# Optimization experiments

Measured on AMD Instinct MI355X. Metric: run time of the kernel, lower is better.

Reference implementation:

```python
import jax, jax.numpy as jnp
import numpy as np

B, S, E, P, H, F = 4, 4096, 256, 32, 8, 1024
DH = E // H
LN_EPS = 1e-5


def setup_inputs() -> dict:
    key = jax.random.key(0)
    ks = jax.random.split(key, 12)
    dt = jnp.float32
    return {
        "src": jax.random.normal(ks[0], (B, S, E), dt),
        "pos_embed": jax.random.normal(ks[1], (B, P, S), dt),
        # learnable positional transform (pos_linear: P -> P)
        "Wpos": jax.random.normal(ks[2], (P, P), dt) * (1.0 / np.sqrt(P)),
        "bpos": jnp.zeros((P,), dt),
        # RBF kernel hyperparameters (ScaleKernel(RBFKernel)) -- positive scalars
        "lengthscale": jnp.full((), 2.0, dt),
        "outputscale": jnp.full((), 1.0, dt),
        # value / output projections of multihead attention
        "Wv": jax.random.normal(ks[3], (E, E), dt) * (1.0 / np.sqrt(E)),
        "bv": jnp.zeros((E,), dt),
        "Wo": jax.random.normal(ks[4], (E, E), dt) * (1.0 / np.sqrt(E)),
        "bo": jnp.zeros((E,), dt),
        # feed-forward
        "W1": jax.random.normal(ks[5], (F, E), dt) * (1.0 / np.sqrt(E)),
        "b1": jnp.zeros((F,), dt),
        "W2": jax.random.normal(ks[6], (E, F), dt) * (1.0 / np.sqrt(F)),
        "b2": jnp.zeros((E,), dt),
        # layer norms
        "ln1_g": jnp.ones((E,), dt), "ln1_b": jnp.zeros((E,), dt),
        "ln2_g": jnp.ones((E,), dt), "ln2_b": jnp.zeros((E,), dt),
    }


def _layer_norm(x, g, b):
    mu = jnp.mean(x, -1, keepdims=True)
    var = jnp.mean(jnp.square(x - mu), -1, keepdims=True)
    return (x - mu) * jax.lax.rsqrt(var + LN_EPS) * g + b


def _rbf_scores(x, lengthscale, outputscale):
    # x: [B, S, P] -> scaled RBF kernel matrix [B, S, S]
    xs = x / lengthscale
    sq = jnp.sum(xs * xs, axis=-1)  # [B, S]
    d2 = sq[:, :, None] + sq[:, None, :] - 2.0 * jnp.einsum('bsp,btp->bst', xs, xs)
    d2 = jnp.maximum(d2, 0.0)
    return outputscale * jnp.exp(-0.5 * d2)


def reference(src, pos_embed, Wpos, bpos, lengthscale, outputscale,
              Wv, bv, Wo, bo, W1, b1, W2, b2, ln1_g, ln1_b, ln2_g, ln2_b):
    b, s, e = src.shape
    # learnable positional transform: [B,P,S] -> [B,S,P] -> linear -> back
    pe = jnp.einsum('bps,op->bos', pos_embed, Wpos) + bpos[None, :, None]  # [B,P,S]
    # GP-kernel attention scores over sequence positions
    scores = _rbf_scores(pe.transpose(0, 2, 1), lengthscale, outputscale)  # [B,S,S]
    attn = jax.nn.softmax(scores, axis=-1)
    # value projection, per-head weighted sum (scores shared across heads)
    v = (src @ Wv.T + bv).reshape(b, s, H, DH)
    ctx = jnp.einsum('bqk,bkhd->bqhd', attn, v).reshape(b, s, e)
    attn_out = ctx @ Wo.T + bo
    x = _layer_norm(src + attn_out, ln1_g, ln1_b)
    ff = jax.nn.relu(x @ W1.T + b1) @ W2.T + b2
    return _layer_norm(x + ff, ln2_g, ln2_b)
```

## Files before the change

### kernel.cpp

```cpp
#include <hip/hip_runtime.h>
#include <stdint.h>

#define BN 4
#define SN 4096
#define EN 256
#define PN 32
#define FN 1024
#define BS (BN*SN)
#define PAUG 64

typedef uint16_t bf16_t;
typedef short v4s  __attribute__((ext_vector_type(4)));
typedef short v8s  __attribute__((ext_vector_type(8)));
typedef __bf16 bf16x8 __attribute__((ext_vector_type(8)));
typedef float v4f   __attribute__((ext_vector_type(4)));
typedef float v16f  __attribute__((ext_vector_type(16)));

#define MFMA16(a,b,c) __builtin_amdgcn_mfma_f32_16x16x32_bf16(a,b,c,0,0,0)
#define MFMA32(a,b,c) __builtin_amdgcn_mfma_f32_32x32x16_bf16(a,b,c,0,0,0)

__device__ __forceinline__ float b2f(bf16_t x){
    uint32_t u = ((uint32_t)x) << 16; float f; __builtin_memcpy(&f, &u, 4); return f;
}
__device__ __forceinline__ bf16_t f2b(float f){
    uint32_t u; __builtin_memcpy(&u, &f, 4);
    u += 0x7FFFu + ((u >> 16) & 1u);
    return (bf16_t)(u >> 16);
}
__device__ __forceinline__ bf16x8 ldb8(const bf16_t* p){
    v8s r = *(const v8s*)p; return __builtin_bit_cast(bf16x8, r);
}
__device__ __forceinline__ bf16x8 ldb8u(const bf16_t* p){
    v4s lo = *(const v4s*)p;
    v4s hi = *(const v4s*)(p + 4);
    v8s r = __builtin_shufflevector(lo, hi, 0,1,2,3,4,5,6,7);
    return __builtin_bit_cast(bf16x8, r);
}
__device__ __forceinline__ float ldsc(const float* p){ return *p; }
__device__ __forceinline__ float ldsc(const bf16_t* p){ return b2f(*p); }
__device__ __forceinline__ void stsc(float* p, float v){ *p = v; }
__device__ __forceinline__ void stsc(bf16_t* p, float v){ *p = f2b(v); }

#if __has_builtin(__builtin_amdgcn_exp2f)
__device__ __forceinline__ float fexp2(float x){ return __builtin_amdgcn_exp2f(x); }
#else
__device__ __forceinline__ float fexp2(float x){ return exp2f(x); }
#endif

#if __has_builtin(__builtin_amdgcn_cvt_pk_bf16_f32)
typedef __bf16 bf16x2 __attribute__((ext_vector_type(2)));
__device__ __forceinline__ uint32_t pkbf16(float a, float b){
    bf16x2 r = __builtin_amdgcn_cvt_pk_bf16_f32(a, b);
    return __builtin_bit_cast(uint32_t, r);
}
#else
__device__ __forceinline__ uint32_t pkbf16(float a, float b){
    return (uint32_t)f2b(a) | ((uint32_t)f2b(b) << 16);
}
#endif

typedef const __attribute__((address_space(1))) uint32_t* glds_gp;
typedef __attribute__((address_space(3))) uint32_t* glds_lp;
__device__ __forceinline__ void glds16(const bf16_t* g, bf16_t* l){
    __builtin_amdgcn_global_load_lds((glds_gp)g, (glds_lp)l, 16, 0, 0);
}

__global__ __launch_bounds__(256) void prep_kernel(
    const float* __restrict__ src, bf16_t* __restrict__ srcb,
    const float* __restrict__ Wv, bf16_t* __restrict__ Wvb,
    const float* __restrict__ Wo, bf16_t* __restrict__ Wob,
    const float* __restrict__ W1, bf16_t* __restrict__ W1b,
    const float* __restrict__ W2, bf16_t* __restrict__ W2b,
    const float* __restrict__ pos, const float* __restrict__ Wp,
    const float* __restrict__ bp,  const float* __restrict__ lsp,
    bf16_t* __restrict__ xk, bf16_t* __restrict__ xq)
{
    __shared__ float Wsh[PN*PN];
    __shared__ float bsh[PN];
    int bid = blockIdx.x;
    int tid = threadIdx.x;

    if (bid < 4736){
        const float* sp; bf16_t* dp; int off;
        if (bid < 4096){ sp = src; dp = srcb; off = (bid*256 + tid)*4; }
        else {
            int i = ((bid - 4096)*256 + tid)*4;
            if      (i <  65536){ sp=Wv; dp=Wvb; off=i; }
            else if (i < 131072){ sp=Wo; dp=Wob; off=i- 65536; }
            else if (i < 393216){ sp=W1; dp=W1b; off=i-131072; }
            else                { sp=W2; dp=W2b; off=i-393216; }
        }
        float4 f = *(const float4*)(sp + off);
        v4s o;
        o.x = (short)f2b(f.x); o.y = (short)f2b(f.y);
        o.z = (short)f2b(f.z); o.w = (short)f2b(f.w);
        *(v4s*)(dp + off) = o;
        return;
    }

    int pb = bid - 4736;
    int b  = pb >> 4;
    int s  = (pb & 15)*256 + tid;

    for (int i = tid; i < PN*PN; i += 256) Wsh[i] = Wp[i];
    if (tid < PN) bsh[tid] = bp[tid];
    __syncthreads();

    float inv_ls = 1.0f / lsp[0];
    const float c1f = 1.4426950408889634f;

    float col[PN];
    #pragma unroll
    for (int p = 0; p < PN; p++) col[p] = pos[((size_t)b*PN + p)*SN + s];

    uint16_t xb[PN], qb[PN];
    float sq = 0.f;
    #pragma unroll 4
    for (int o = 0; o < PN; o++){
        float pe = bsh[o];
        #pragma unroll
        for (int p = 0; p < PN; p++) pe += col[p] * Wsh[o*PN + p];
        float pv = pe * inv_ls;
        uint16_t h = f2b(pv);
        xb[o] = h;
        qb[o] = f2b(c1f * pv);
        float xr = b2f(h);
        sq += xr * xr;
    }

    size_t base = ((size_t)b*SN + s) * PAUG;
    v8s pk[8];
    #pragma unroll
    for (int c = 0; c < 4; c++)
        #pragma unroll
        for (int j = 0; j < 8; j++) ((short*)&pk[c])[j] = (short)xb[c*8 + j];
    #pragma unroll
    for (int c = 4; c < 8; c++)
        #pragma unroll
        for (int j = 0; j < 8; j++) ((short*)&pk[c])[j] = 0;
    ((short*)&pk[4])[0] = (short)f2b(-0.5f * sq);
    ((short*)&pk[4])[1] = (short)0x3F80;
    #pragma unroll
    for (int c = 0; c < 8; c++) *(v8s*)(xk + base + c*8) = pk[c];

    #pragma unroll
    for (int c = 0; c < 4; c++)
        #pragma unroll
        for (int j = 0; j < 8; j++) ((short*)&pk[c])[j] = (short)qb[c*8 + j];
    ((short*)&pk[4])[0] = (short)f2b(c1f);
    ((short*)&pk[4])[1] = (short)f2b(-0.5f * sq * c1f);
    #pragma unroll
    for (int c = 0; c < 8; c++) *(v8s*)(xq + base + c*8) = pk[c];
}

template<int EPI, typename OutT>
__global__ __launch_bounds__(256) void gemm_t(
    const bf16_t* __restrict__ A, const bf16_t* __restrict__ W,
    const float* __restrict__ bias, OutT* __restrict__ out,
    bf16_t* __restrict__ vt, int N, int K)
{
    __shared__ __align__(16) bf16_t At[2][4096];
    __shared__ __align__(16) bf16_t Wt[2][4096];
    int tid = threadIdx.x;
    int lane = tid & 63, wv = tid >> 6, col = lane & 15, quad = lane >> 4;
    int m0 = blockIdx.x * 64, n0 = blockIdx.y * 64;
    int nck = K >> 6;

    int srow = tid >> 3;
    int spc  = (tid & 7) ^ (srow & 7);
    const bf16_t* asrc = A + (size_t)(m0 + srow)*K + spc*8;
    const bf16_t* wsrc = W + (size_t)(n0 + srow)*K + spc*8;

    v4f acc[4];
    #pragma unroll
    for (int t = 0; t < 4; t++) acc[t] = (v4f){0.f,0.f,0.f,0.f};

    glds16(asrc, &At[0][tid*8]);
    glds16(asrc + (size_t)32*K, &At[0][2048 + tid*8]);
    glds16(wsrc, &Wt[0][tid*8]);
    glds16(wsrc + (size_t)32*K, &Wt[0][2048 + tid*8]);
    __syncthreads();

    for (int c = 0; c < nck; c++){
        int cb = c & 1;
        if (c + 1 < nck){
            glds16(asrc + (c+1)*64, &At[cb^1][tid*8]);
            glds16(asrc + (size_t)32*K + (c+1)*64, &At[cb^1][2048 + tid*8]);
            glds16(wsrc + (c+1)*64, &Wt[cb^1][tid*8]);
            glds16(wsrc + (size_t)32*K + (c+1)*64, &Wt[cb^1][2048 + tid*8]);
        }
        #pragma unroll
        for (int kc = 0; kc < 2; kc++){
            int pc = ((kc*4 + quad) ^ (col & 7)) * 8;
            bf16x8 a = ldb8(&At[cb][(wv*16 + col)*64 + pc]);
            #pragma unroll
            for (int t = 0; t < 4; t++){
                bf16x8 b = ldb8(&Wt[cb][(t*16 + col)*64 + pc]);
                acc[t] = MFMA16(a, b, acc[t]);
            }
        }
        __syncthreads();
    }

    float bfv[4];
    #pragma unroll
    for (int t = 0; t < 4; t++) bfv[t] = bias[n0 + t*16 + col];

    if constexpr (EPI == 3){
        __shared__ uint16_t Tsh[64*74];
        #pragma unroll
        for (int r = 0; r < 4; r++)
            #pragma unroll
            for (int t = 0; t < 4; t++)
                Tsh[(wv*16 + quad*4 + r)*74 + t*16 + col] = f2b(acc[t][r] + bfv[t]);
        __syncthreads();
        int e = tid >> 2, sc = tid & 3;
        int b = m0 >> 12;
        int sbat = m0 & (SN-1);
        int eb   = (n0 + e) >> 5;
        int l31e = (n0 + e) & 31;
        int k16  = (sbat >> 4) + sc;
        v8s p0, p1;
        #pragma unroll
        for (int i = 0; i < 8; i++) ((short*)&p0)[i] = (short)Tsh[(sc*16 + i)*74 + e];
        #pragma unroll
        for (int i = 0; i < 8; i++) ((short*)&p1)[i] = (short)Tsh[(sc*16 + 8 + i)*74 + e];
        bf16_t* dst = vt + ((((size_t)b*8 + eb)*256 + k16)*64 + l31e)*8;
        *(v8s*)dst = p0;
        *(v8s*)(dst + 256) = p1;
    } else {
        #pragma unroll
        for (int r = 0; r < 4; r++){
            int row = m0 + wv*16 + quad*4 + r;
            #pragma unroll
            for (int t = 0; t < 4; t++){
                float y = acc[t][r] + bfv[t];
                if constexpr (EPI == 1) y = fmaxf(y, 0.f);
                stsc(out + (size_t)row*N + n0 + t*16 + col, y);
            }
        }
    }
}

template<typename OutT, typename ResT>
__global__ __launch_bounds__(256) void ln_kernel(
    const bf16_t* __restrict__ y, const ResT* __restrict__ res,
    const float* __restrict__ gamma, const float* __restrict__ beta,
    OutT* __restrict__ out)
{
    int tid = threadIdx.x;
    int row = blockIdx.x * 32 + (tid >> 3);
    int l8  = tid & 7;
    size_t base = (size_t)row * EN;
    float v[32];
    float s1 = 0.f, s2 = 0.f;
    #pragma unroll
    for (int i = 0; i < 4; i++){
        int off = l8*8 + i*64;
        v8s a = *(const v8s*)(y + base + off);
        #pragma unroll
        for (int j = 0; j < 8; j++){
            float t = b2f((bf16_t)(uint16_t)a[j]) + ldsc(res + base + off + j);
            v[i*8 + j] = t; s1 += t; s2 += t*t;
        }
    }
    #pragma unroll
    for (int m = 1; m <= 4; m <<= 1){
        s1 += __shfl_xor(s1, m);
        s2 += __shfl_xor(s2, m);
    }
    float mu = s1 * (1.f/256.f);
    float rs = rsqrtf(s2 * (1.f/256.f) - mu*mu + 1e-5f);
    #pragma unroll
    for (int i = 0; i < 4; i++){
        int off = l8*8 + i*64;
        #pragma unroll
        for (int j = 0; j < 8; j++)
            stsc(out + base + off + j, (v[i*8+j]-mu)*rs*gamma[off+j] + beta[off+j]);
    }
}

__global__ __launch_bounds__(512, 2) void attn_kernel(
    const bf16_t* __restrict__ xk, const bf16_t* __restrict__ xq,
    const bf16_t* __restrict__ vf, const float* __restrict__ osp,
    bf16_t* __restrict__ ctx)
{
    __shared__ __align__(16) bf16_t Wtb[2][64*260];
    __shared__ __align__(16) bf16_t Qs[64*64];
    __shared__ float densh[8][64];
    __shared__ float dent[64];

    int tid  = threadIdx.x;
    int lane = tid & 63;
    int wv   = tid >> 6;
    int col  = lane & 15;
    int quad = lane >> 4;
    int l31  = lane & 31;
    int half = lane >> 5;

    int bid = blockIdx.x;
    int b   = (bid & 7) >> 1;
    int qi  = ((bid >> 3) << 1) | (bid & 1);
    int q0  = qi * 64;

    float k2 = 1.4426950408889634f * osp[0];

    const bf16_t* xkb = xk + (size_t)b * SN * PAUG;
    const bf16_t* xqb = xq + (size_t)b * SN * PAUG;
    const bf16_t* vfb = vf + (((size_t)b*8 + wv)*256)*512 + lane*8;

    {
        int qrow = tid >> 3;
        int qpc  = (tid & 7) ^ (qrow & 7);
        glds16(xqb + (size_t)(q0 + qrow)*PAUG + qpc*8, &Qs[tid*8]);
    }

    v16f acc[2];
    #pragma unroll
    for (int qg = 0; qg < 2; qg++)
        #pragma unroll
        for (int i = 0; i < 16; i++) acc[qg][i] = 0.f;
    float den[4] = {0.f, 0.f, 0.f, 0.f};
    const v4f zero = (v4f){0.f,0.f,0.f,0.f};

    bf16x8 kf[2][2];
    #pragma unroll
    for (int kg = 0; kg < 2; kg++)
        #pragma unroll
        for (int h = 0; h < 2; h++)
            kf[kg][h] = ldb8(xkb + (size_t)(wv*32 + kg*16 + col)*PAUG + h*32 + quad*8);

    __syncthreads();

    for (int c = 0; c < 16; c++){
        int cb = c & 1;
        bf16x8 vr[16];
        #pragma unroll
        for (int sk = 0; sk < 16; sk++)
            vr[sk] = ldb8(vfb + (size_t)(c*16 + sk)*512);

        #pragma unroll
        for (int qg = 0; qg < 2; qg++){
            #pragma unroll
            for (int g2 = 0; g2 < 2; g2++){
                int qr = qg*32 + g2*16 + col;
                bf16x8 qa = ldb8(&Qs[qr*64 + ((quad    ) ^ (col & 7))*8]);
                bf16x8 qb = ldb8(&Qs[qr*64 + ((4 + quad) ^ (col & 7))*8]);
                #pragma unroll
                for (int kg = 0; kg < 2; kg++){
                    v4f st = MFMA16(kf[kg][0], qa, zero);
                    st = MFMA16(kf[kg][1], qb, st);
                    #pragma unroll
                    for (int rp = 0; rp < 2; rp++){
                        float w0 = fexp2(fmaf(k2, fexp2(st[rp*2+0]), -k2));
                        float w1 = fexp2(fmaf(k2, fexp2(st[rp*2+1]), -k2));
                        den[qg*2+g2] += w0 + w1;
                        *(uint32_t*)&Wtb[cb][qr*260 + wv*32 + kg*16 + quad*4 + rp*2]
                            = pkbf16(w0, w1);
                    }
                }
            }
        }
        __syncthreads();

        if (c + 1 < 16){
            #pragma unroll
            for (int kg = 0; kg < 2; kg++)
                #pragma unroll
                for (int h = 0; h < 2; h++)
                    kf[kg][h] = ldb8(xkb + (size_t)((c+1)*256 + wv*32 + kg*16 + col)*PAUG
                                     + h*32 + quad*8);
        }

        #pragma unroll
        for (int qg = 0; qg < 2; qg++){
            #pragma unroll
            for (int sk4 = 0; sk4 < 4; sk4++){
                bf16x8 af[4];
                #pragma unroll
                for (int j = 0; j < 4; j++)
                    af[j] = ldb8u(&Wtb[cb][(qg*32 + l31)*260 + (sk4*4 + j)*16 + half*8]);
                #pragma unroll
                for (int j = 0; j < 4; j++)
                    acc[qg] = MFMA32(af[j], vr[sk4*4 + j], acc[qg]);
            }
        }
    }

    #pragma unroll
    for (int d = 0; d < 4; d++){
        den[d] += __shfl_xor(den[d], 16);
        den[d] += __shfl_xor(den[d], 32);
    }
    if (lane < 16){
        #pragma unroll
        for (int qg = 0; qg < 2; qg++)
            #pragma unroll
            for (int g2 = 0; g2 < 2; g2++)
                densh[wv][qg*32 + g2*16 + lane] = den[qg*2+g2];
    }
    __syncthreads();
    if (tid < 64){
        float s = 0.f;
        #pragma unroll
        for (int w = 0; w < 8; w++) s += densh[w][tid];
        dent[tid] = 1.f / s;
    }
    __syncthreads();

    size_t obase = ((size_t)b*SN + q0) * EN + wv*32;
    #pragma unroll
    for (int qg = 0; qg < 2; qg++){
        #pragma unroll
        for (int rg = 0; rg < 16; rg++){
            int row = (rg & 3) + 8*(rg >> 2) + 4*half;
            float inv = dent[qg*32 + row];
            ctx[obase + (size_t)(qg*32 + row)*EN + l31] = f2b(acc[qg][rg] * inv);
        }
    }
}

extern "C" void kernel_launch(void* const* d_in, const int* in_sizes, int n_in,
                              void* d_out, int out_size, void* d_ws, size_t ws_size,
                              hipStream_t stream)
{
    (void)in_sizes; (void)n_in; (void)out_size; (void)ws_size;
    const float* src  = (const float*)d_in[0];
    const float* pos  = (const float*)d_in[1];
    const float* Wpos = (const float*)d_in[2];
    const float* bpos = (const float*)d_in[3];
    const float* ls   = (const float*)d_in[4];
    const float* os   = (const float*)d_in[5];
    const float* Wv   = (const float*)d_in[6];
    const float* bv   = (const float*)d_in[7];
    const float* Wo   = (const float*)d_in[8];
    const float* bo   = (const float*)d_in[9];
    const float* W1   = (const float*)d_in[10];
    const float* b1   = (const float*)d_in[11];
    const float* W2   = (const float*)d_in[12];
    const float* b2   = (const float*)d_in[13];
    const float* g1   = (const float*)d_in[14];
    const float* be1  = (const float*)d_in[15];
    const float* g2   = (const float*)d_in[16];
    const float* be2  = (const float*)d_in[17];

    char* w = (char*)d_ws;
    bf16_t* xkb  = (bf16_t*)(w);
    bf16_t* xqb  = (bf16_t*)(w + ( 2u<<20));
    bf16_t* Wvb  = (bf16_t*)(w + ( 4u<<20));
    bf16_t* Wob  = (bf16_t*)(w + ( 4u<<20) + (1u<<18));
    bf16_t* W1b  = (bf16_t*)(w + ( 5u<<20));
    bf16_t* W2b  = (bf16_t*)(w + ( 6u<<20));
    bf16_t* srcb = (bf16_t*)(w + ( 8u<<20));
    bf16_t* y2   = (bf16_t*)(w + ( 8u<<20));
    bf16_t* vtg  = (bf16_t*)(w + (16u<<20));
    bf16_t* y1   = (bf16_t*)(w + (16u<<20));
    bf16_t* ctx  = (bf16_t*)(w + (24u<<20));
    bf16_t* xws  = (bf16_t*)(w + (24u<<20));
    bf16_t* hws  = (bf16_t*)(w + (32u<<20));

    prep_kernel<<<dim3(4800), 256, 0, stream>>>(
        src, srcb, Wv, Wvb, Wo, Wob, W1, W1b, W2, W2b,
        pos, Wpos, bpos, ls, xkb, xqb);

    gemm_t<3, bf16_t><<<dim3(BS/64, EN/64), 256, 0, stream>>>(
        srcb, Wvb, bv, (bf16_t*)nullptr, vtg, EN, EN);
    attn_kernel<<<dim3(256), 512, 0, stream>>>(xkb, xqb, vtg, os, ctx);
    gemm_t<0, bf16_t><<<dim3(BS/64, EN/64), 256, 0, stream>>>(
        ctx, Wob, bo, y1, (bf16_t*)nullptr, EN, EN);
    ln_kernel<bf16_t, bf16_t><<<dim3(BS/32), 256, 0, stream>>>(y1, srcb, g1, be1, xws);
    gemm_t<1, bf16_t><<<dim3(BS/64, FN/64), 256, 0, stream>>>(
        xws, W1b, b1, hws, (bf16_t*)nullptr, FN, EN);
    gemm_t<0, bf16_t><<<dim3(BS/64, EN/64), 256, 0, stream>>>(
        hws, W2b, b2, y2, (bf16_t*)nullptr, EN, FN);
    ln_kernel<float, bf16_t><<<dim3(BS/32), 256, 0, stream>>>(y2, xws, g2, be2, (float*)d_out);
}
```

Baseline: 243.0 us.

## Split attention kernel across 16 waves with key-half partitioning and cross-wave reduction

Doubles the attention block to 1024 threads. Each wave now computes score weights for 16 keys instead of 32, and in the PV phase each pair of waves (kh 0/1) covers half of the key chunk for the same 32 output columns. The two partial accumulators are summed through shared memory at the end. The chunk loop is unrolled by two with ping-pong K-fragment registers and an explicit waitcnt/barrier. The aim is more in-flight waves and less per-wave register pressure to hide latency, at the cost of an extra LDS reduction and higher per-block resource demand.

```diff
diff --git a/kernel.cpp b/kernel.cpp
--- a/kernel.cpp
+++ b/kernel.cpp
@@ -280,14 +280,14 @@
     }
 }
 
-__global__ __launch_bounds__(512, 2) void attn_kernel(
+__global__ __launch_bounds__(1024, 4) void attn_kernel(
     const bf16_t* __restrict__ xk, const bf16_t* __restrict__ xq,
     const bf16_t* __restrict__ vf, const float* __restrict__ osp,
     bf16_t* __restrict__ ctx)
 {
     __shared__ __align__(16) bf16_t Wtb[2][64*260];
     __shared__ __align__(16) bf16_t Qs[64*64];
-    __shared__ float densh[8][64];
+    __shared__ float densh[16][64];
     __shared__ float dent[64];
 
     int tid  = threadIdx.x;
@@ -297,6 +297,8 @@
     int quad = lane >> 4;
     int l31  = lane & 31;
     int half = lane >> 5;
+    int es   = wv & 7;
+    int kh   = wv >> 3;
 
     int bid = blockIdx.x;
     int b   = (bid & 7) >> 1;
@@ -307,9 +309,9 @@
 
     const bf16_t* xkb = xk + (size_t)b * SN * PAUG;
     const bf16_t* xqb = xq + (size_t)b * SN * PAUG;
-    const bf16_t* vfb = vf + (((size_t)b*8 + wv)*256)*512 + lane*8;
-
-    {
+    const bf16_t* vfb = vf + (((size_t)b*8 + es)*256)*512 + lane*8;
+
+    if (tid < 512){
         int qrow = tid >> 3;
         int qpc  = (tid & 7) ^ (qrow & 7);
         glds16(xqb + (size_t)(q0 + qrow)*PAUG + qpc*8, &Qs[tid*8]);
@@ -323,69 +325,75 @@
     float den[4] = {0.f, 0.f, 0.f, 0.f};
     const v4f zero = (v4f){0.f,0.f,0.f,0.f};
 
-    bf16x8 kf[2][2];
-    #pragma unroll
-    for (int kg = 0; kg < 2; kg++)
-        #pragma unroll
-        for (int h = 0; h < 2; h++)
-            kf[kg][h] = ldb8(xkb + (size_t)(wv*32 + kg*16 + col)*PAUG + h*32 + quad*8);
-
     __syncthreads();
 
-    for (int c = 0; c < 16; c++){
-        int cb = c & 1;
-        bf16x8 vr[16];
-        #pragma unroll
-        for (int sk = 0; sk < 16; sk++)
-            vr[sk] = ldb8(vfb + (size_t)(c*16 + sk)*512);
-
-        #pragma unroll
-        for (int qg = 0; qg < 2; qg++){
-            #pragma unroll
-            for (int g2 = 0; g2 < 2; g2++){
-                int qr = qg*32 + g2*16 + col;
-                bf16x8 qa = ldb8(&Qs[qr*64 + ((quad    ) ^ (col & 7))*8]);
-                bf16x8 qb = ldb8(&Qs[qr*64 + ((4 + quad) ^ (col & 7))*8]);
-                #pragma unroll
-                for (int kg = 0; kg < 2; kg++){
-                    v4f st = MFMA16(kf[kg][0], qa, zero);
-                    st = MFMA16(kf[kg][1], qb, st);
-                    #pragma unroll
-                    for (int rp = 0; rp < 2; rp++){
-                        float w0 = fexp2(fmaf(k2, fexp2(st[rp*2+0]), -k2));
-                        float w1 = fexp2(fmaf(k2, fexp2(st[rp*2+1]), -k2));
-                        den[qg*2+g2] += w0 + w1;
-                        *(uint32_t*)&Wtb[cb][qr*260 + wv*32 + kg*16 + quad*4 + rp*2]
-                            = pkbf16(w0, w1);
-                    }
-                }
-            }
-        }
-        __syncthreads();
-
-        if (c + 1 < 16){
-            #pragma unroll
-            for (int kg = 0; kg < 2; kg++)
-                #pragma unroll
-                for (int h = 0; h < 2; h++)
-                    kf[kg][h] = ldb8(xkb + (size_t)((c+1)*256 + wv*32 + kg*16 + col)*PAUG
-                                     + h*32 + quad*8);
-        }
-
-        #pragma unroll
-        for (int qg = 0; qg < 2; qg++){
-            #pragma unroll
-            for (int sk4 = 0; sk4 < 4; sk4++){
-                bf16x8 af[4];
-                #pragma unroll
-                for (int j = 0; j < 4; j++)
-                    af[j] = ldb8u(&Wtb[cb][(qg*32 + l31)*260 + (sk4*4 + j)*16 + half*8]);
-                #pragma unroll
-                for (int j = 0; j < 4; j++)
-                    acc[qg] = MFMA32(af[j], vr[sk4*4 + j], acc[qg]);
-            }
-        }
-    }
+    bf16x8 kfA[2], kfB[2], vr[8];
+    {
+        const bf16_t* kr = xkb + (size_t)(wv*16 + col)*PAUG + quad*8;
+        kfA[0] = ldb8(kr); kfA[1] = ldb8(kr + 32);
+    }
+    #pragma unroll
+    for (int sk = 0; sk < 8; sk++)
+        vr[sk] = ldb8(vfb + (size_t)(kh*8 + sk)*512);
+
+#define CHUNK_BODY(CC, PAR, KFC, KFN)                                          \
+  {                                                                            \
+                                \
+    _Pragma("unroll")                                                          \
+    for (int qg = 0; qg < 2; qg++){                                            \
+      _Pragma("unroll")                                                        \
+      for (int g2 = 0; g2 < 2; g2++){                                          \
+        int qr = qg*32 + g2*16 + col;                                          \
+        bf16x8 qa = ldb8(&Qs[qr*64 + ((quad    ) ^ (col & 7))*8]);             \
+        bf16x8 qb = ldb8(&Qs[qr*64 + ((4 + quad) ^ (col & 7))*8]);             \
+        v4f st = MFMA16(KFC[0], qa, zero);                                     \
+        st = MFMA16(KFC[1], qb, st);                                           \
+        _Pragma("unroll")                                                      \
+        for (int rp = 0; rp < 2; rp++){                                        \
+          float w0 = fexp2(fmaf(k2, fexp2(st[rp*2+0]), -k2));                  \
+          float w1 = fexp2(fmaf(k2, fexp2(st[rp*2+1]), -k2));                  \
+          den[qg*2+g2] += w0 + w1;                                             \
+          *(uint32_t*)&Wtb[PAR][qr*260 + wv*16 + quad*4 + rp*2]                \
+              = pkbf16(w0, w1);                                                \
+        }                                                                      \
+      }                                                                        \
+    }                                                                          \
+                     \
+    if ((CC) + 1 < 16){                                                        \
+      const bf16_t* kr_ = xkb + (size_t)(((CC)+1)*256 + wv*16 + col)*PAUG + quad*8; \
+      KFN[0] = ldb8(kr_); KFN[1] = ldb8(kr_ + 32);                             \
+    }                                                                          \
+    asm volatile("s_waitcnt lgkmcnt(0)" ::: "memory");                         \
+    __builtin_amdgcn_s_barrier();                                              \
+    __builtin_amdgcn_sched_barrier(0);                                         \
+                       \
+    _Pragma("unroll")                                                          \
+    for (int qg = 0; qg < 2; qg++){                                            \
+      _Pragma("unroll")                                                        \
+      for (int sk4 = 0; sk4 < 2; sk4++){                                       \
+        bf16x8 af[4];                                                          \
+        _Pragma("unroll")                                                      \
+        for (int j = 0; j < 4; j++)                                            \
+          af[j] = ldb8u(&Wtb[PAR][(qg*32 + l31)*260 + kh*128 + (sk4*4 + j)*16 + half*8]); \
+        _Pragma("unroll")                                                      \
+        for (int j = 0; j < 4; j++)                                            \
+          acc[qg] = MFMA32(af[j], vr[sk4*4 + j], acc[qg]);                     \
+      }                                                                        \
+    }                                                                          \
+                 \
+    if ((CC) + 1 < 16){                                                        \
+      _Pragma("unroll")                                                        \
+      for (int sk = 0; sk < 8; sk++)                                           \
+        vr[sk] = ldb8(vfb + (size_t)((((CC)+1)*16) + kh*8 + sk)*512);          \
+    }                                                                          \
+  }
+
+    #pragma unroll 1
+    for (int cc = 0; cc < 16; cc += 2){
+        CHUNK_BODY(cc,     0, kfA, kfB);
+        CHUNK_BODY(cc + 1, 1, kfB, kfA);
+    }
+#undef CHUNK_BODY
 
     #pragma unroll
     for (int d = 0; d < 4; d++){
@@ -400,22 +408,35 @@
                 densh[wv][qg*32 + g2*16 + lane] = den[qg*2+g2];
     }
     __syncthreads();
+
+    float* Csh = (float*)&Wtb[0][0];
+    if (kh == 1){
+        #pragma unroll
+        for (int qg = 0; qg < 2; qg++)
+            #pragma unroll
+            for (int rg = 0; rg < 16; rg++){
+                int row = (rg & 3) + 8*(rg >> 2) + 4*half;
+                Csh[es*2048 + (qg*32 + row)*32 + l31] = acc[qg][rg];
+            }
+    }
     if (tid < 64){
         float s = 0.f;
         #pragma unroll
-        for (int w = 0; w < 8; w++) s += densh[w][tid];
+        for (int w = 0; w < 16; w++) s += densh[w][tid];
         dent[tid] = 1.f / s;
     }
     __syncthreads();
 
-    size_t obase = ((size_t)b*SN + q0) * EN + wv*32;
-    #pragma unroll
-    for (int qg = 0; qg < 2; qg++){
-        #pragma unroll
-        for (int rg = 0; rg < 16; rg++){
-            int row = (rg & 3) + 8*(rg >> 2) + 4*half;
-            float inv = dent[qg*32 + row];
-            ctx[obase + (size_t)(qg*32 + row)*EN + l31] = f2b(acc[qg][rg] * inv);
+    if (kh == 0){
+        size_t obase = ((size_t)b*SN + q0) * EN + es*32;
+        #pragma unroll
+        for (int qg = 0; qg < 2; qg++){
+            #pragma unroll
+            for (int rg = 0; rg < 16; rg++){
+                int row = (rg & 3) + 8*(rg >> 2) + 4*half;
+                float v = acc[qg][rg] + Csh[es*2048 + (qg*32 + row)*32 + l31];
+                ctx[obase + (size_t)(qg*32 + row)*EN + l31] = f2b(v * dent[qg*32 + row]);
+            }
         }
     }
 }
@@ -465,7 +486,7 @@
 
     gemm_t<3, bf16_t><<<dim3(BS/64, EN/64), 256, 0, stream>>>(
         srcb, Wvb, bv, (bf16_t*)nullptr, vtg, EN, EN);
-    attn_kernel<<<dim3(256), 512, 0, stream>>>(xkb, xqb, vtg, os, ctx);
+    attn_kernel<<<dim3(256), 1024, 0, stream>>>(xkb, xqb, vtg, os, ctx);
     gemm_t<0, bf16_t><<<dim3(BS/64, EN/64), 256, 0, stream>>>(
         ctx, Wob, bo, y1, (bf16_t*)nullptr, EN, EN);
     ln_kernel<bf16_t, bf16_t><<<dim3(BS/32), 256, 0, stream>>>(y1, srcb, g1, be1, xws);
```

Measured after the change: 251.3 us. 1.03x slower.

## Halve attention key chunk to 128 to cut registers and LDS, raise occupancy

Applied to the files above, without the earlier changes.

The attention kernel now handles 128 keys per iteration instead of 256. Each wave owns one 16-key group, holds half as many value fragments, and uses a half-sized score buffer, which lets launch bounds request 4 blocks per CU instead of 2. The generic syncthreads is replaced by an explicit lgkmcnt wait, raw barrier and scheduling barrier, with the next key prefetch placed before it. Twice as many loop iterations and barriers are added in exchange for higher occupancy and latency hiding, and register pressure under the tighter bound may cause spills.

```diff
diff --git a/kernel.cpp b/kernel.cpp
--- a/kernel.cpp
+++ b/kernel.cpp
@@ -280,12 +280,12 @@
     }
 }
 
-__global__ __launch_bounds__(512, 2) void attn_kernel(
+__global__ __launch_bounds__(512, 4) void attn_kernel(
     const bf16_t* __restrict__ xk, const bf16_t* __restrict__ xq,
     const bf16_t* __restrict__ vf, const float* __restrict__ osp,
     bf16_t* __restrict__ ctx)
 {
-    __shared__ __align__(16) bf16_t Wtb[2][64*260];
+    __shared__ __align__(16) bf16_t Wtb[2][64*132];
     __shared__ __align__(16) bf16_t Qs[64*64];
     __shared__ float densh[8][64];
     __shared__ float dent[64];
@@ -323,21 +323,20 @@
     float den[4] = {0.f, 0.f, 0.f, 0.f};
     const v4f zero = (v4f){0.f,0.f,0.f,0.f};
 
-    bf16x8 kf[2][2];
-    #pragma unroll
-    for (int kg = 0; kg < 2; kg++)
-        #pragma unroll
-        for (int h = 0; h < 2; h++)
-            kf[kg][h] = ldb8(xkb + (size_t)(wv*32 + kg*16 + col)*PAUG + h*32 + quad*8);
+    bf16x8 kf0, kf1;
+    {
+        const bf16_t* kr = xkb + (size_t)(wv*16 + col)*PAUG + quad*8;
+        kf0 = ldb8(kr); kf1 = ldb8(kr + 32);
+    }
 
     __syncthreads();
 
-    for (int c = 0; c < 16; c++){
+    for (int c = 0; c < 32; c++){
         int cb = c & 1;
-        bf16x8 vr[16];
-        #pragma unroll
-        for (int sk = 0; sk < 16; sk++)
-            vr[sk] = ldb8(vfb + (size_t)(c*16 + sk)*512);
+        bf16x8 vr[8];
+        #pragma unroll
+        for (int sk = 0; sk < 8; sk++)
+            vr[sk] = ldb8(vfb + (size_t)(c*8 + sk)*512);
 
         #pragma unroll
         for (int qg = 0; qg < 2; qg++){
@@ -346,40 +345,36 @@
                 int qr = qg*32 + g2*16 + col;
                 bf16x8 qa = ldb8(&Qs[qr*64 + ((quad    ) ^ (col & 7))*8]);
                 bf16x8 qb = ldb8(&Qs[qr*64 + ((4 + quad) ^ (col & 7))*8]);
+                v4f st = MFMA16(kf0, qa, zero);
+                st = MFMA16(kf1, qb, st);
                 #pragma unroll
-                for (int kg = 0; kg < 2; kg++){
-                    v4f st = MFMA16(kf[kg][0], qa, zero);
-                    st = MFMA16(kf[kg][1], qb, st);
-                    #pragma unroll
-                    for (int rp = 0; rp < 2; rp++){
-                        float w0 = fexp2(fmaf(k2, fexp2(st[rp*2+0]), -k2));
-                        float w1 = fexp2(fmaf(k2, fexp2(st[rp*2+1]), -k2));
-                        den[qg*2+g2] += w0 + w1;
-                        *(uint32_t*)&Wtb[cb][qr*260 + wv*32 + kg*16 + quad*4 + rp*2]
-                            = pkbf16(w0, w1);
-                    }
+                for (int rp = 0; rp < 2; rp++){
+                    float w0 = fexp2(fmaf(k2, fexp2(st[rp*2+0]), -k2));
+                    float w1 = fexp2(fmaf(k2, fexp2(st[rp*2+1]), -k2));
+                    den[qg*2+g2] += w0 + w1;
+                    *(uint32_t*)&Wtb[cb][qr*132 + wv*16 + quad*4 + rp*2]
+                        = pkbf16(w0, w1);
                 }
             }
         }
-        __syncthreads();
-
-        if (c + 1 < 16){
-            #pragma unroll
-            for (int kg = 0; kg < 2; kg++)
-                #pragma unroll
-                for (int h = 0; h < 2; h++)
-                    kf[kg][h] = ldb8(xkb + (size_t)((c+1)*256 + wv*32 + kg*16 + col)*PAUG
-                                     + h*32 + quad*8);
-        }
+
+        if (c + 1 < 32){
+            const bf16_t* kr = xkb + (size_t)((c+1)*128 + wv*16 + col)*PAUG + quad*8;
+            kf0 = ldb8(kr); kf1 = ldb8(kr + 32);
+        }
+
+        asm volatile("s_waitcnt lgkmcnt(0)" ::: "memory");
+        __builtin_amdgcn_s_barrier();
+        __builtin_amdgcn_sched_barrier(0);
 
         #pragma unroll
         for (int qg = 0; qg < 2; qg++){
             #pragma unroll
-            for (int sk4 = 0; sk4 < 4; sk4++){
+            for (int sk4 = 0; sk4 < 2; sk4++){
                 bf16x8 af[4];
                 #pragma unroll
                 for (int j = 0; j < 4; j++)
-                    af[j] = ldb8u(&Wtb[cb][(qg*32 + l31)*260 + (sk4*4 + j)*16 + half*8]);
+                    af[j] = ldb8u(&Wtb[cb][(qg*32 + l31)*132 + (sk4*4 + j)*16 + half*8]);
                 #pragma unroll
                 for (int j = 0; j < 4; j++)
                     acc[qg] = MFMA32(af[j], vr[sk4*4 + j], acc[qg]);
```

New measurement: 246.1 us. About the same (+1.3%).
